# Performance work log

Hardware: AMD Instinct MI355X
Metric: run time of the kernel (lower is better)

Reference implementation:

```python
import jax, jax.numpy as jnp
import numpy as np

B, S, D, H = 2, 2048, 1024, 16
HD = D // H  # head_dim = 64
ROPE_BASE = 10000.0
NEG_MIN = jnp.finfo(jnp.float32).min


def _rope_cos_sin(seq_len, head_dim):
    inv_freq = 1.0 / (ROPE_BASE ** (jnp.arange(0, head_dim, 2, dtype=jnp.float32) / head_dim))
    t = jnp.arange(seq_len, dtype=jnp.float32)
    freqs = jnp.einsum('i,j->ij', t, inv_freq)           # [S, HD/2]
    emb = jnp.concatenate([freqs, freqs], axis=-1)        # [S, HD]
    return jnp.cos(emb), jnp.sin(emb)


def _rotate_half(x):
    x1, x2 = jnp.split(x, 2, axis=-1)
    return jnp.concatenate([-x2, x1], axis=-1)


def setup_inputs() -> dict:
    key = jax.random.key(0)
    ks = jax.random.split(key, 5)
    sc = 0.02
    hidden_states = jax.random.normal(ks[0], (B, S, D), dtype=jnp.float32)
    wq = jax.random.normal(ks[1], (D, D), dtype=jnp.float32) * sc
    wk = jax.random.normal(ks[2], (D, D), dtype=jnp.float32) * sc
    wv = jax.random.normal(ks[3], (D, D), dtype=jnp.float32) * sc
    wo = jax.random.normal(ks[4], (D, D), dtype=jnp.float32) * sc
    # additive causal mask [B,1,S,S]: 0 on/below diagonal, large negative above
    causal = jnp.tril(jnp.ones((S, S), dtype=jnp.bool_))
    attention_mask = jnp.where(causal, 0.0, NEG_MIN)[None, None, :, :].astype(jnp.float32)
    attention_mask = jnp.broadcast_to(attention_mask, (B, 1, S, S))
    position_ids = jnp.broadcast_to(jnp.arange(S, dtype=jnp.int32)[None, :], (B, S))
    return {"hidden_states": hidden_states, "attention_mask": attention_mask,
            "wq": wq, "wk": wk, "wv": wv, "wo": wo, "position_ids": position_ids}


def reference(hidden_states, attention_mask, wq, wk, wv, wo, position_ids):
    bsz, q_len, _ = hidden_states.shape

    def shape_heads(x):
        return x.reshape(bsz, q_len, H, HD).transpose(0, 2, 1, 3)  # [B,H,S,HD]

    q = shape_heads(hidden_states @ wq)
    k = shape_heads(hidden_states @ wk)
    v = shape_heads(hidden_states @ wv)

    cos, sin = _rope_cos_sin(q_len, HD)                   # [S, HD]
    cos = cos[position_ids][:, None, :, :]                # [B,1,S,HD]
    sin = sin[position_ids][:, None, :, :]
    q = q * cos + _rotate_half(q) * sin
    k = k * cos + _rotate_half(k) * sin

    scores = jnp.einsum('bhqd,bhkd->bhqk', q, k) / jnp.sqrt(jnp.float32(HD))
    scores = jnp.maximum(scores + attention_mask, NEG_MIN)
    attn = jax.nn.softmax(scores, axis=-1)
    out = jnp.einsum('bhqk,bhkd->bhqd', attn, v)          # [B,H,S,HD]
    out = out.transpose(0, 2, 1, 3).reshape(bsz, q_len, D)
    return out @ wo
```

## Files before the change

kernel.cpp:

```cpp
#include <hip/hip_runtime.h>
#include <hip/hip_bf16.h>

#define B_ 2
#define S_ 2048
#define D_ 1024
#define H_ 16
#define HD_ 64

typedef unsigned short u16;
typedef __attribute__((ext_vector_type(8))) short short8;
typedef __attribute__((ext_vector_type(4))) float f32x4;

#if __has_builtin(__builtin_amdgcn_exp2f)
#define EXP2F(x) __builtin_amdgcn_exp2f(x)
#else
#define EXP2F(x) exp2f(x)
#endif

__device__ __forceinline__ u16 f2bf(float f) {
  union { float f; unsigned u; } v; v.f = f;
  unsigned r = v.u + 0x7fffu + ((v.u >> 16) & 1u);
  return (u16)(r >> 16);
}
__device__ __forceinline__ unsigned pkbf(float a, float b) {
  union { __hip_bfloat162 h; unsigned u; } v;
  v.h = __float22bfloat162_rn(float2{a, b});
  return v.u;
}
__device__ __forceinline__ void gload_lds16(const u16* g, u16* l) {
  __builtin_amdgcn_global_load_lds((const __attribute__((address_space(1))) void*)g,
                                   (__attribute__((address_space(3))) void*)l, 16, 0, 0);
}

__global__ __launch_bounds__(256) void prep_kernel(const float* __restrict__ hs,
                                                   const float* __restrict__ W0,
                                                   const float* __restrict__ W1,
                                                   const float* __restrict__ W2,
                                                   const float* __restrict__ W3,
                                                   u16* __restrict__ Xb,
                                                   u16* __restrict__ WT) {
  __shared__ float T[64][65];
  if (blockIdx.z == 4) {
    const int base = (blockIdx.y * 16 + blockIdx.x) * 4096 + threadIdx.x;
#pragma unroll 4
    for (int i = 0; i < 16; ++i) {
      const int idx = base + i * 256;
      const float4 v = ((const float4*)hs)[idx];
      ushort4 o;
      o.x = f2bf(v.x); o.y = f2bf(v.y); o.z = f2bf(v.z); o.w = f2bf(v.w);
      ((ushort4*)Xb)[idx] = o;
    }
    return;
  }
  const float* Wz[4] = {W0, W1, W2, W3};
  const float* W = Wz[blockIdx.z];
  u16* dst = WT + (size_t)blockIdx.z * (1024 * 1024);
  const int nb = blockIdx.x * 64, kb = blockIdx.y * 64;
  const int t = threadIdx.x;
  const int r = t >> 2, c4 = (t & 3) * 16;
#pragma unroll
  for (int i = 0; i < 4; ++i) {
    float4 v = *(const float4*)&W[(kb + r) * D_ + nb + c4 + i * 4];
    T[r][c4 + i * 4 + 0] = v.x;
    T[r][c4 + i * 4 + 1] = v.y;
    T[r][c4 + i * 4 + 2] = v.z;
    T[r][c4 + i * 4 + 3] = v.w;
  }
  __syncthreads();
#pragma unroll
  for (int i = 0; i < 4; ++i) {
    ushort4 o;
    o.x = f2bf(T[c4 + i * 4 + 0][r]);
    o.y = f2bf(T[c4 + i * 4 + 1][r]);
    o.z = f2bf(T[c4 + i * 4 + 2][r]);
    o.w = f2bf(T[c4 + i * 4 + 3][r]);
    *(ushort4*)&dst[(nb + r) * D_ + kb + c4 + i * 4] = o;
  }
}

template <int BN, int MODE, int DB>
__global__ __launch_bounds__(256) void gemm_kernel(const u16* __restrict__ A,
                                                   const u16* __restrict__ BT,
                                                   float* __restrict__ out0,
                                                   u16* __restrict__ oQ,
                                                   u16* __restrict__ oK,
                                                   u16* __restrict__ oV,
                                                   const int* __restrict__ posarr) {
  constexpr int K = D_;
  constexpr int NT = BN / 32;
  constexpr int BI = BN / 32;
  constexpr int ABANK = 128 * 64;
  constexpr int BBANK = BN * 64;
  constexpr int STAGE = (DB + 1) * (ABANK + BBANK);
  constexpr int EPIU = (MODE == 1) ? 128 * 136 : 0;
  constexpr int SMU = STAGE > EPIU ? STAGE : EPIU;
  __shared__ u16 smem[SMU];
  u16* AsP = smem;
  u16* BsP = smem + (DB + 1) * ABANK;

  const int t = threadIdx.x, lane = t & 63, w = t >> 6;
  const int l15 = lane & 15, quad = lane >> 4;
  const int flat = blockIdx.x;
  const int xcd = flat & 7, j = flat >> 3;
  const int m0 = ((xcd << 2) + (j & 3)) * 128;
  const int n0 = (j >> 2) * BN;
  const int wm = (w >> 1) * 64, wn = (w & 1) * (BN / 2);

  f32x4 acc[4][NT];
#pragma unroll
  for (int mt = 0; mt < 4; ++mt)
#pragma unroll
    for (int nt = 0; nt < NT; ++nt) acc[mt][nt] = (f32x4){0.f, 0.f, 0.f, 0.f};

  const u16* ag[4]; int aoff[4];
  const u16* bg[BI]; int boff[BI];
#pragma unroll
  for (int jj = 0; jj < 4; ++jj) {
    int slot = w * 256 + jj * 64 + lane;
    int row = slot >> 3, q = (slot & 7) ^ (row & 7);
    ag[jj] = A + (size_t)(m0 + row) * K + q * 8;
    aoff[jj] = (w * 256 + jj * 64) * 8;
  }
#pragma unroll
  for (int jj = 0; jj < BI; ++jj) {
    int slot = w * (BI * 64) + jj * 64 + lane;
    int row = slot >> 3, q = (slot & 7) ^ (row & 7);
    bg[jj] = BT + (size_t)(n0 + row) * K + q * 8;
    boff[jj] = (w * (BI * 64) + jj * 64) * 8;
  }

  auto stage = [&](int k0, int buf) {
#pragma unroll
    for (int jj = 0; jj < 4; ++jj) gload_lds16(ag[jj] + k0, AsP + buf * ABANK + aoff[jj]);
#pragma unroll
    for (int jj = 0; jj < BI; ++jj) gload_lds16(bg[jj] + k0, BsP + buf * BBANK + boff[jj]);
  };
  auto compute = [&](int buf) {
    const u16* Ab = AsP + buf * ABANK;
    const u16* Bb = BsP + buf * BBANK;
#pragma unroll
    for (int kc = 0; kc < 2; ++kc) {
      short8 af[4], bf[NT];
#pragma unroll
      for (int mt = 0; mt < 4; ++mt) {
        int row = wm + mt * 16 + l15;
        af[mt] = *(const short8*)&Ab[row * 64 + (((kc * 4 + quad) ^ (row & 7)) * 8)];
      }
#pragma unroll
      for (int nt = 0; nt < NT; ++nt) {
        int col = wn + nt * 16 + l15;
        bf[nt] = *(const short8*)&Bb[col * 64 + (((kc * 4 + quad) ^ (col & 7)) * 8)];
      }
#pragma unroll
      for (int mt = 0; mt < 4; ++mt)
#pragma unroll
        for (int nt = 0; nt < NT; ++nt)
          acc[mt][nt] = __builtin_amdgcn_mfma_f32_16x16x32_bf16(af[mt], bf[nt], acc[mt][nt], 0, 0, 0);
    }
  };

  if constexpr (DB == 0) {
    for (int k0 = 0; k0 < K; k0 += 64) {
      __syncthreads();
      stage(k0, 0);
      __syncthreads();
      compute(0);
    }
  } else {
    stage(0, 0);
#pragma unroll 1
    for (int it = 0; it < K / 64; ++it) {
      __syncthreads();
      if (it + 1 < K / 64) stage((it + 1) * 64, (it + 1) & 1);
      compute(it & 1);
    }
  }

  if (MODE == 0) {
#pragma unroll
    for (int mt = 0; mt < 4; ++mt) {
      const int row0 = m0 + wm + mt * 16 + quad * 4;
#pragma unroll
      for (int nt = 0; nt < NT; ++nt) {
        const int col = n0 + wn + nt * 16 + l15;
#pragma unroll
        for (int r = 0; r < 4; ++r) out0[(size_t)(row0 + r) * 1024 + col] = acc[mt][nt][r];
      }
    }
  } else {
    const int widx = n0 >> 10;
    if (widx == 2) {
      __syncthreads();
      u16* Epi = smem;
#pragma unroll
      for (int nt = 0; nt < NT; ++nt) {
        const int col = wn + nt * 16 + l15;
#pragma unroll
        for (int mt = 0; mt < 4; ++mt) {
          const int row0 = wm + mt * 16 + quad * 4;
          uint2 pk;
          pk.x = pkbf(acc[mt][nt][0], acc[mt][nt][1]);
          pk.y = pkbf(acc[mt][nt][2], acc[mt][nt][3]);
          *(uint2*)&Epi[col * 136 + row0] = pk;
        }
      }
      __syncthreads();
      const int col = t >> 1, half = t & 1;
      const int cc = (n0 + col) & 1023;
      const int h = cc >> 6, d = cc & 63;
      const int bb = m0 >> 11;
      const int s0 = (m0 & (S_ - 1)) + half * 64;
      u16* gp = oV + ((((size_t)(bb * H_ + h) * HD_ + d)) << 11) + s0;
#pragma unroll
      for (int i = 0; i < 8; ++i)
        ((uint4*)gp)[i] = *(const uint4*)&Epi[col * 136 + half * 64 + i * 8];
    } else {
      u16* dst = (widx == 0) ? oQ : oK;
      const float scale = (widx == 0) ? 0.18033688011f : 1.0f;
      float invf[2];
      invf[0] = exp2f(-0.41524101186f * (float)l15);
      invf[1] = exp2f(-0.41524101186f * (float)(16 + l15));
      __syncthreads();
      u16* Epi = smem;
#pragma unroll
      for (int mt = 0; mt < 4; ++mt) {
        const int lrow0 = wm + mt * 16 + quad * 4;
#pragma unroll
        for (int r = 0; r < 4; ++r) {
          const int rw = m0 + lrow0 + r;
          const int b = rw >> 11, s = rw & (S_ - 1);
          const float pos = (float)posarr[b * S_ + s];
#pragma unroll
          for (int nt2 = 0; nt2 < 2; ++nt2) {
            float sn, c;
            __sincosf(pos * invf[nt2], &sn, &c);
            const float x1 = acc[mt][nt2][r], x2 = acc[mt][nt2 + 2][r];
            const int d = nt2 * 16 + l15;
            Epi[(lrow0 + r) * 136 + wn + d] = f2bf((x1 * c - x2 * sn) * scale);
            Epi[(lrow0 + r) * 136 + wn + d + 32] = f2bf((x2 * c + x1 * sn) * scale);
          }
        }
      }
      __syncthreads();
      const int bb = m0 >> 11, s0 = m0 & (S_ - 1);
      const int sl = t >> 1, d0 = (t & 1) * 32;
#pragma unroll
      for (int hh = 0; hh < 2; ++hh) {
        const int h = ((n0 + hh * 64) & 1023) >> 6;
        u16* gp = dst + (((size_t)(bb * H_ + h) * S_ + s0 + sl) << 6) + d0;
#pragma unroll
        for (int k2 = 0; k2 < 4; ++k2)
          ((uint4*)gp)[k2] = *(const uint4*)&Epi[sl * 136 + hh * 64 + d0 + k2 * 8];
      }
    }
  }
}

__global__ __launch_bounds__(256, 2) void attn_kernel(const u16* __restrict__ Q,
                                                      const u16* __restrict__ Kx,
                                                      const u16* __restrict__ Vt,
                                                      u16* __restrict__ AO) {
  __shared__ u16 Ks[2][2][512 * 8];
  __shared__ u16 Vs[2][2][512 * 8];
  __shared__ u16 Pw[4][128 * 8];
  const int t = threadIdx.x;
  const int lane = t & 63, w = t >> 6;
  const int l15 = lane & 15, quad = lane >> 4;
  const int idx = blockIdx.x;
  const int pr = (idx >> 3) & 15;
  const int bh = (idx & 7) | ((idx >> 7) << 3);
  const int qtA = pr, qtB = 31 - pr;
  const u16* qp = Q + bh * (S_ * HD_);
  const u16* kp = Kx + bh * (S_ * HD_);
  const u16* vp = Vt + bh * (HD_ * S_);
  const int wq16 = w * 16;
  const int q_loA = qtA * 64 + wq16;
  const int q_loB = qtB * 64 + wq16;

  int srow[2], sq[2];
#pragma unroll
  for (int jj = 0; jj < 2; ++jj) {
    int slot = w * 128 + jj * 64 + lane;
    srow[jj] = slot >> 3;
    sq[jj] = (slot & 7) ^ (srow[jj] & 7);
  }
  auto stageT = [&](int kt, int buf, int tt) {
#pragma unroll
    for (int jj = 0; jj < 2; ++jj)
      gload_lds16(kp + (size_t)(kt * 64 + srow[jj]) * 64 + sq[jj] * 8,
                  &Ks[buf][tt][(w * 128 + jj * 64) * 8]);
#pragma unroll
    for (int jj = 0; jj < 2; ++jj)
      gload_lds16(vp + (size_t)srow[jj] * S_ + kt * 64 + sq[jj] * 8,
                  &Vs[buf][tt][(w * 128 + jj * 64) * 8]);
  };
  auto stageGroup = [&](int g, int buf, int ktmax) {
    const int kt0 = g * 2;
    stageT(kt0, buf, 0);
    if (kt0 + 1 <= ktmax) stageT(kt0 + 1, buf, 1);
  };

  short8 qfA[2], qfB[2];
#pragma unroll
  for (int kc = 0; kc < 2; ++kc) {
    qfA[kc] = *(const short8*)&qp[(q_loA + l15) * HD_ + kc * 32 + quad * 8];
    qfB[kc] = *(const short8*)&qp[(q_loB + l15) * HD_ + kc * 32 + quad * 8];
  }

  f32x4 oA[4], oB[4];
  float mA = -INFINITY, lA = 0.f, mB = -INFINITY, lB = 0.f;
#pragma unroll
  for (int i = 0; i < 4; ++i) {
    oA[i] = (f32x4){0.f, 0.f, 0.f, 0.f};
    oB[i] = (f32x4){0.f, 0.f, 0.f, 0.f};
  }

  auto chainStep = [&](bool diag, const short8* qf, const short8* kf, const short8* vf,
                       f32x4* o, float& m_, float& l_) {
    f32x4 sa[4];
#pragma unroll
    for (int i = 0; i < 4; ++i) sa[i] = (f32x4){0.f, 0.f, 0.f, 0.f};
#pragma unroll
    for (int kc = 0; kc < 2; ++kc)
#pragma unroll
      for (int nt = 0; nt < 4; ++nt)
        sa[nt] = __builtin_amdgcn_mfma_f32_16x16x32_bf16(kf[kc * 4 + nt], qf[kc], sa[nt], 0, 0, 0);
    if (diag) {
#pragma unroll
      for (int nt = 0; nt < 4; ++nt)
#pragma unroll
        for (int r = 0; r < 4; ++r)
          if (nt * 16 + quad * 4 + r > wq16 + l15) sa[nt][r] = -INFINITY;
    }
    float mx = -INFINITY;
#pragma unroll
    for (int nt = 0; nt < 4; ++nt)
#pragma unroll
      for (int r = 0; r < 4; ++r) mx = fmaxf(mx, sa[nt][r]);
    mx = fmaxf(mx, __shfl_xor(mx, 16));
    mx = fmaxf(mx, __shfl_xor(mx, 32));
    const float mn = fmaxf(m_, mx);
    const float alpha = EXP2F(m_ - mn);
    m_ = mn;
    float p[16];
    float sum = 0.f;
#pragma unroll
    for (int nt = 0; nt < 4; ++nt)
#pragma unroll
      for (int r = 0; r < 4; ++r) {
        const float pe = EXP2F(sa[nt][r] - mn);
        p[nt * 4 + r] = pe;
        sum += pe;
      }
    sum += __shfl_xor(sum, 16);
    sum += __shfl_xor(sum, 32);
    l_ = l_ * alpha + sum;
#pragma unroll
    for (int dt = 0; dt < 4; ++dt)
#pragma unroll
      for (int r = 0; r < 4; ++r) o[dt][r] *= alpha;
#pragma unroll
    for (int nt = 0; nt < 4; ++nt) {
      const int q = nt * 2 + (quad >> 1);
      uint2 pk;
      pk.x = pkbf(p[nt * 4 + 0], p[nt * 4 + 1]);
      pk.y = pkbf(p[nt * 4 + 2], p[nt * 4 + 3]);
      *(uint2*)&Pw[w][(l15 * 8 + (q ^ (l15 & 7))) * 8 + (quad & 1) * 4] = pk;
    }
#pragma unroll
    for (int kc = 0; kc < 2; ++kc) {
      short8 pf = *(const short8*)&Pw[w][(l15 * 8 + (((kc * 4) + quad) ^ (l15 & 7))) * 8];
#pragma unroll
      for (int dt = 0; dt < 4; ++dt)
        o[dt] = __builtin_amdgcn_mfma_f32_16x16x32_bf16(vf[dt * 2 + kc], pf, o[dt], 0, 0, 0);
    }
  };

  auto loadFrags = [&](int buf, int tt, short8* kf, short8* vf) {
#pragma unroll
    for (int kc = 0; kc < 2; ++kc)
#pragma unroll
      for (int nt = 0; nt < 4; ++nt) {
        const int row = nt * 16 + l15;
        kf[kc * 4 + nt] =
            *(const short8*)&Ks[buf][tt][(row * 8 + ((kc * 4 + quad) ^ (row & 7))) * 8];
      }
#pragma unroll
    for (int dt = 0; dt < 4; ++dt)
#pragma unroll
      for (int kc = 0; kc < 2; ++kc) {
        const int row = dt * 16 + l15;
        vf[dt * 2 + kc] =
            *(const short8*)&Vs[buf][tt][(row * 8 + ((kc * 4 + quad) ^ (row & 7))) * 8];
      }
  };

  const int ktmax = qtB;
  const int ngroups = (ktmax + 2) >> 1;
  short8 kf[8], vf[8];
  stageGroup(0, 0, ktmax);
#pragma unroll 1
  for (int g = 0; g < ngroups; ++g) {
    __syncthreads();
    if (g + 1 < ngroups) stageGroup(g + 1, (g + 1) & 1, ktmax);
    const int buf = g & 1;
    const int kt0 = 2 * g;
    loadFrags(buf, 0, kf, vf);
    chainStep(kt0 == qtB, qfB, kf, vf, oB, mB, lB);
    if (kt0 <= qtA) chainStep(kt0 == qtA, qfA, kf, vf, oA, mA, lA);
    if (kt0 + 1 <= ktmax) {
      loadFrags(buf, 1, kf, vf);
      chainStep(kt0 + 1 == qtB, qfB, kf, vf, oB, mB, lB);
      if (kt0 + 1 <= qtA) chainStep(kt0 + 1 == qtA, qfA, kf, vf, oA, mA, lA);
    }
  }

  const int b = bh >> 4, h = bh & 15;
  const float liA = 1.0f / lA, liB = 1.0f / lB;
  const size_t baseA = ((size_t)(b * S_ + q_loA + l15)) * D_ + h * HD_;
  const size_t baseB = ((size_t)(b * S_ + q_loB + l15)) * D_ + h * HD_;
#pragma unroll
  for (int dt = 0; dt < 4; ++dt)
#pragma unroll
    for (int rr = 0; rr < 2; ++rr) {
      *(unsigned*)&AO[baseA + dt * 16 + quad * 4 + rr * 2] =
          pkbf(oA[dt][rr * 2] * liA, oA[dt][rr * 2 + 1] * liA);
      *(unsigned*)&AO[baseB + dt * 16 + quad * 4 + rr * 2] =
          pkbf(oB[dt][rr * 2] * liB, oB[dt][rr * 2 + 1] * liB);
    }
}

extern "C" void kernel_launch(void* const* d_in, const int* in_sizes, int n_in,
                              void* d_out, int out_size, void* d_ws, size_t ws_size,
                              hipStream_t stream) {
  const float* hs = (const float*)d_in[0];
  const float* wq = (const float*)d_in[2];
  const float* wk = (const float*)d_in[3];
  const float* wv = (const float*)d_in[4];
  const float* wo = (const float*)d_in[5];
  const int* pos = (const int*)d_in[6];
  float* out = (float*)d_out;

  char* ws = (char*)d_ws;
  const size_t MB = (size_t)1 << 20;
  u16* Xb = (u16*)(ws);
  u16* WT = (u16*)(ws + 8 * MB);
  u16* Qh = (u16*)(ws + 16 * MB);
  u16* Kh = (u16*)(ws + 24 * MB);
  u16* Vt = (u16*)(ws + 32 * MB);
  u16* AO = (u16*)(ws + 40 * MB);

  prep_kernel<<<dim3(16, 16, 5), 256, 0, stream>>>(hs, wq, wk, wv, wo, Xb, WT);

  gemm_kernel<128, 1, 0><<<768, 256, 0, stream>>>(Xb, WT, nullptr, Qh, Kh, Vt, pos);

  attn_kernel<<<512, 256, 0, stream>>>(Qh, Kh, Vt, AO);

  gemm_kernel<64, 0, 1><<<512, 256, 0, stream>>>(AO, WT + 3 * 1024 * 1024, out,
                                                 nullptr, nullptr, nullptr, nullptr);
}
```

Baseline: 205.5 us.

## Use triple-buffered BK=32 async LDS pipeline with vmcnt waits in GEMMs

Measured after the change: 201.1 us. 1.02x faster.

```diff
diff --git a/kernel.cpp b/kernel.cpp
--- a/kernel.cpp
+++ b/kernel.cpp
@@ -78,7 +78,7 @@
   }
 }
 
-template <int BN, int MODE, int DB>
+template <int BN, int MODE>
 __global__ __launch_bounds__(256) void gemm_kernel(const u16* __restrict__ A,
                                                    const u16* __restrict__ BT,
                                                    float* __restrict__ out0,
@@ -87,16 +87,16 @@
                                                    u16* __restrict__ oV,
                                                    const int* __restrict__ posarr) {
   constexpr int K = D_;
+  constexpr int BK = 32;
+  constexpr int NSTEP = K / BK;
   constexpr int NT = BN / 32;
-  constexpr int BI = BN / 32;
-  constexpr int ABANK = 128 * 64;
-  constexpr int BBANK = BN * 64;
-  constexpr int STAGE = (DB + 1) * (ABANK + BBANK);
+  constexpr int NBR = (BN * BK) / 2048;
+  constexpr int ABANK = 128 * BK;
+  constexpr int BBANK = BN * BK;
+  constexpr int BUFSZ = ABANK + BBANK;
   constexpr int EPIU = (MODE == 1) ? 128 * 136 : 0;
-  constexpr int SMU = STAGE > EPIU ? STAGE : EPIU;
+  constexpr int SMU = (3 * BUFSZ > EPIU) ? 3 * BUFSZ : EPIU;
   __shared__ u16 smem[SMU];
-  u16* AsP = smem;
-  u16* BsP = smem + (DB + 1) * ABANK;
 
   const int t = threadIdx.x, lane = t & 63, w = t >> 6;
   const int l15 = lane & 15, quad = lane >> 4;
@@ -112,69 +112,81 @@
 #pragma unroll
     for (int nt = 0; nt < NT; ++nt) acc[mt][nt] = (f32x4){0.f, 0.f, 0.f, 0.f};
 
-  const u16* ag[4]; int aoff[4];
-  const u16* bg[BI]; int boff[BI];
-#pragma unroll
-  for (int jj = 0; jj < 4; ++jj) {
-    int slot = w * 256 + jj * 64 + lane;
-    int row = slot >> 3, q = (slot & 7) ^ (row & 7);
-    ag[jj] = A + (size_t)(m0 + row) * K + q * 8;
-    aoff[jj] = (w * 256 + jj * 64) * 8;
-  }
-#pragma unroll
-  for (int jj = 0; jj < BI; ++jj) {
-    int slot = w * (BI * 64) + jj * 64 + lane;
-    int row = slot >> 3, q = (slot & 7) ^ (row & 7);
-    bg[jj] = BT + (size_t)(n0 + row) * K + q * 8;
-    boff[jj] = (w * (BI * 64) + jj * 64) * 8;
+  const u16* agp[2]; int adst[2];
+  const u16* bgp[NBR]; int bdst[NBR];
+#pragma unroll
+  for (int jj = 0; jj < 2; ++jj) {
+    const int slot = jj * 256 + w * 64 + lane;
+    const int row = slot >> 2, c = slot & 3, q = c ^ ((row >> 1) & 3);
+    agp[jj] = A + (size_t)(m0 + row) * K + q * 8;
+    adst[jj] = (jj * 256 + w * 64) * 8;
+  }
+#pragma unroll
+  for (int jj = 0; jj < NBR; ++jj) {
+    const int slot = jj * 256 + w * 64 + lane;
+    const int row = slot >> 2, c = slot & 3, q = c ^ ((row >> 1) & 3);
+    bgp[jj] = BT + (size_t)(n0 + row) * K + q * 8;
+    bdst[jj] = ABANK + (jj * 256 + w * 64) * 8;
   }
 
   auto stage = [&](int k0, int buf) {
-#pragma unroll
-    for (int jj = 0; jj < 4; ++jj) gload_lds16(ag[jj] + k0, AsP + buf * ABANK + aoff[jj]);
-#pragma unroll
-    for (int jj = 0; jj < BI; ++jj) gload_lds16(bg[jj] + k0, BsP + buf * BBANK + boff[jj]);
-  };
+    u16* base = smem + buf * BUFSZ;
+#pragma unroll
+    for (int jj = 0; jj < 2; ++jj) gload_lds16(agp[jj] + k0, base + adst[jj]);
+#pragma unroll
+    for (int jj = 0; jj < NBR; ++jj) gload_lds16(bgp[jj] + k0, base + bdst[jj]);
+  };
+
+  int afo[4], bfo[NT];
+#pragma unroll
+  for (int mt = 0; mt < 4; ++mt) {
+    const int row = wm + mt * 16 + l15;
+    afo[mt] = row * BK + (quad ^ ((row >> 1) & 3)) * 8;
+  }
+#pragma unroll
+  for (int nt = 0; nt < NT; ++nt) {
+    const int col = wn + nt * 16 + l15;
+    bfo[nt] = ABANK + col * BK + (quad ^ ((col >> 1) & 3)) * 8;
+  }
+
   auto compute = [&](int buf) {
-    const u16* Ab = AsP + buf * ABANK;
-    const u16* Bb = BsP + buf * BBANK;
-#pragma unroll
-    for (int kc = 0; kc < 2; ++kc) {
-      short8 af[4], bf[NT];
-#pragma unroll
-      for (int mt = 0; mt < 4; ++mt) {
-        int row = wm + mt * 16 + l15;
-        af[mt] = *(const short8*)&Ab[row * 64 + (((kc * 4 + quad) ^ (row & 7)) * 8)];
-      }
-#pragma unroll
-      for (int nt = 0; nt < NT; ++nt) {
-        int col = wn + nt * 16 + l15;
-        bf[nt] = *(const short8*)&Bb[col * 64 + (((kc * 4 + quad) ^ (col & 7)) * 8)];
-      }
-#pragma unroll
-      for (int mt = 0; mt < 4; ++mt)
-#pragma unroll
-        for (int nt = 0; nt < NT; ++nt)
-          acc[mt][nt] = __builtin_amdgcn_mfma_f32_16x16x32_bf16(af[mt], bf[nt], acc[mt][nt], 0, 0, 0);
-    }
-  };
-
-  if constexpr (DB == 0) {
-    for (int k0 = 0; k0 < K; k0 += 64) {
-      __syncthreads();
-      stage(k0, 0);
-      __syncthreads();
-      compute(0);
-    }
-  } else {
-    stage(0, 0);
+    const u16* base = smem + buf * BUFSZ;
+    short8 af[4], bf[NT];
+#pragma unroll
+    for (int mt = 0; mt < 4; ++mt) af[mt] = *(const short8*)&base[afo[mt]];
+#pragma unroll
+    for (int nt = 0; nt < NT; ++nt) bf[nt] = *(const short8*)&base[bfo[nt]];
+#pragma unroll
+    for (int mt = 0; mt < 4; ++mt)
+#pragma unroll
+      for (int nt = 0; nt < NT; ++nt)
+        acc[mt][nt] = __builtin_amdgcn_mfma_f32_16x16x32_bf16(af[mt], bf[nt], acc[mt][nt], 0, 0, 0);
+  };
+
+  stage(0, 0);
+  stage(BK, 1);
+  int bc = 0, bs = 2;
 #pragma unroll 1
-    for (int it = 0; it < K / 64; ++it) {
-      __syncthreads();
-      if (it + 1 < K / 64) stage((it + 1) * 64, (it + 1) & 1);
-      compute(it & 1);
-    }
-  }
+  for (int it = 0; it < NSTEP - 2; ++it) {
+    if constexpr (MODE == 1) asm volatile("s_waitcnt vmcnt(4)" ::: "memory");
+    else                     asm volatile("s_waitcnt vmcnt(3)" ::: "memory");
+    __builtin_amdgcn_s_barrier();
+    __builtin_amdgcn_sched_barrier(0);
+    stage((it + 2) * BK, bs);
+    compute(bc);
+    bc = bc == 2 ? 0 : bc + 1;
+    bs = bs == 2 ? 0 : bs + 1;
+  }
+  if constexpr (MODE == 1) asm volatile("s_waitcnt vmcnt(4)" ::: "memory");
+  else                     asm volatile("s_waitcnt vmcnt(3)" ::: "memory");
+  __builtin_amdgcn_s_barrier();
+  __builtin_amdgcn_sched_barrier(0);
+  compute(bc);
+  bc = bc == 2 ? 0 : bc + 1;
+  asm volatile("s_waitcnt vmcnt(0)" ::: "memory");
+  __builtin_amdgcn_s_barrier();
+  __builtin_amdgcn_sched_barrier(0);
+  compute(bc);
 
   if (MODE == 0) {
 #pragma unroll
@@ -452,10 +464,10 @@
 
   prep_kernel<<<dim3(16, 16, 5), 256, 0, stream>>>(hs, wq, wk, wv, wo, Xb, WT);
 
-  gemm_kernel<128, 1, 0><<<768, 256, 0, stream>>>(Xb, WT, nullptr, Qh, Kh, Vt, pos);
+  gemm_kernel<128, 1><<<768, 256, 0, stream>>>(Xb, WT, nullptr, Qh, Kh, Vt, pos);
 
   attn_kernel<<<512, 256, 0, stream>>>(Qh, Kh, Vt, AO);
 
-  gemm_kernel<64, 0, 1><<<512, 256, 0, stream>>>(AO, WT + 3 * 1024 * 1024, out,
-                                                 nullptr, nullptr, nullptr, nullptr);
-}
+  gemm_kernel<64, 0><<<512, 256, 0, stream>>>(AO, WT + 3 * 1024 * 1024, out,
+                                              nullptr, nullptr, nullptr, nullptr);
+}
```
